# Performance work log

Hardware: AMD Instinct MI355X
Metric: run time of the kernel (lower is better)

Reference implementation:

```python
import jax, jax.numpy as jnp
import numpy as np

TILE = 16            # TILE_WIDTH == TILE_HEIGHT in the Taichi kernel
H, W = 512, 512
TV, TU = H // TILE, W // TILE
NT = TV * TU         # number of 16x16 tiles
PPT = 64             # depth-sorted points assigned to each tile (uniform/padded)
N = NT * PPT


def setup_inputs() -> dict:
    key = jax.random.key(0)
    ks = jax.random.split(key, 7)
    # each tile owns a contiguous depth-sorted chunk of the global point list
    tile_of_point = jnp.arange(N) // PPT
    tu = (tile_of_point % TU).astype(jnp.float32)
    tv = (tile_of_point // TU).astype(jnp.float32)
    center = jnp.stack([tu * TILE + TILE / 2, tv * TILE + TILE / 2], -1)
    point_uv = center + jax.random.normal(ks[0], (N, 2)) * 6.0
    # conic = inverse 2x2 covariance packed as [a, b, c]; keep positive definite
    a = jax.random.uniform(ks[1], (N,), minval=0.02, maxval=0.3)
    c = jax.random.uniform(ks[2], (N,), minval=0.02, maxval=0.3)
    b = jax.random.uniform(ks[3], (N,), minval=-0.5, maxval=0.5) * jnp.sqrt(a * c)
    point_uv_conic = jnp.stack([a, b, c], -1)
    point_alpha_after_activation = jax.random.uniform(ks[4], (N,))
    point_color = jax.random.uniform(ks[5], (N, 3))
    # depths sorted within each tile chunk (front-to-back order, as after radix sort)
    point_depth = jnp.sort(
        jax.random.uniform(ks[6], (N,), minval=0.5, maxval=50.0).reshape(NT, PPT), axis=-1
    ).reshape(N)
    tile_point_indices = jnp.arange(N, dtype=jnp.int32).reshape(NT, PPT)
    return dict(point_uv=point_uv, point_uv_conic=point_uv_conic,
                point_alpha_after_activation=point_alpha_after_activation,
                point_color=point_color, point_depth=point_depth,
                tile_point_indices=tile_point_indices,
                camera_height=H, camera_width=W)


def _to_image(x, tv, tu):
    # x: [NT, TILE*TILE, ...] -> [H, W, ...] (tiles row-major, pixels row-major in tile)
    rest = x.shape[2:]
    x = x.reshape(tv, tu, TILE, TILE, *rest)
    x = jnp.swapaxes(x, 1, 2)
    return x.reshape(tv * TILE, tu * TILE, *rest)


def reference(point_uv, point_uv_conic, point_alpha_after_activation, point_color,
              point_depth, tile_point_indices, camera_height, camera_width):
    TU_ = camera_width // TILE
    TV_ = camera_height // TILE
    NT_ = TU_ * TV_
    PPT_ = tile_point_indices.shape[1]
    # gather per-tile point attributes: [NT, PPT, ...]
    g_uv = point_uv[tile_point_indices]
    g_conic = point_uv_conic[tile_point_indices]
    g_alpha = point_alpha_after_activation[tile_point_indices]
    g_color = point_color[tile_point_indices]
    g_depth = point_depth[tile_point_indices]
    # pixel centers for every tile: [NT, 256]
    p = jnp.arange(TILE * TILE)
    tid = jnp.arange(NT_)
    pix_u = (tid % TU_)[:, None].astype(jnp.float32) * TILE + (p % TILE).astype(jnp.float32)[None, :] + 0.5
    pix_v = (tid // TU_)[:, None].astype(jnp.float32) * TILE + (p // TILE).astype(jnp.float32)[None, :] + 0.5
    # Gaussian density from conic: exp(-0.5*(a dx^2 + c dy^2) - b dx dy)  [NT, 256, PPT]
    dx = pix_u[:, :, None] - g_uv[:, None, :, 0]
    dy = pix_v[:, :, None] - g_uv[:, None, :, 1]
    ca = g_conic[:, None, :, 0]; cb = g_conic[:, None, :, 1]; cc = g_conic[:, None, :, 2]
    dens = jnp.exp(-0.5 * (ca * dx * dx + cc * dy * dy) - cb * dx * dy)
    alpha = dens * g_alpha[:, None, :]
    visible = alpha >= 1.0 / 255.0           # kernel: continue if alpha < 1/255
    alpha_c = jnp.where(visible, jnp.minimum(alpha, 0.99), 0.0)
    one_m = 1.0 - alpha_c
    cp = jnp.cumprod(one_m, axis=-1)
    Ti = jnp.concatenate([jnp.ones_like(cp[..., :1]), cp[..., :-1]], axis=-1)  # exclusive transmittance
    # point whose next_T < 1e-4 saturates the pixel and is itself skipped
    trigger = visible & (Ti * one_m < 1e-4)
    saturated = jnp.cumsum(trigger.astype(jnp.int32), axis=-1) > 0
    contributes = visible & ~saturated
    w = jnp.where(contributes, alpha_c * Ti, 0.0)   # per-point compositing weight
    acc_color = jnp.einsum('tpk,tkc->tpc', w, g_color)
    norm = jnp.sum(w, axis=-1)
    acc_depth = jnp.sum(w * g_depth[:, None, :], axis=-1)
    T_final = jnp.prod(jnp.where(contributes, one_m, 1.0), axis=-1)
    valid_count = jnp.sum(contributes, axis=-1).astype(jnp.int32)
    j = jnp.arange(PPT_, dtype=jnp.int32)
    last = jnp.max(jnp.where(contributes, j[None, None, :] + 1, 0), axis=-1)
    last_offset = (jnp.arange(NT_, dtype=jnp.int32) * PPT_)[:, None] + last
    rasterized_image = _to_image(acc_color, TV_, TU_)
    rasterized_depth = _to_image(acc_depth / jnp.maximum(norm, 1e-6), TV_, TU_)
    pixel_accumulated_alpha = _to_image(1.0 - T_final, TV_, TU_)
    pixel_offset_of_last_effective_point = _to_image(last_offset, TV_, TU_)
    pixel_valid_point_count = _to_image(valid_count, TV_, TU_)
    return (rasterized_image, rasterized_depth, pixel_accumulated_alpha,
            pixel_offset_of_last_effective_point, pixel_valid_point_count)
```

## Files before the change

### kernel.cpp

```cpp
#include <hip/hip_runtime.h>

#define TILE 16
#define PPT 64

#if __has_builtin(__builtin_amdgcn_exp2f)
#define EXP2F(x) __builtin_amdgcn_exp2f(x)
#else
#define EXP2F(x) exp2f(x)
#endif

__device__ __forceinline__ int read_dim(const int* p) {
    int v = *p;
    if (v >= TILE && v <= 65536 && (v % TILE) == 0) return v;
    float f = __int_as_float(v);
    return (int)f;
}

struct Acc {
    float T, Tg, r, g, b, d;
    int cnt, last;
};

__device__ __forceinline__ void step(
    float e, float alpha, const float4& C, int jp1, Acc& a)
{
    const bool  vis   = e >= -7.9943533f;
    const float one_m = fmaxf(1.0f - alpha, 0.01f);
    const float Tone  = a.Tg * one_m;
    const bool  contrib = vis && (Tone >= 1e-4f);
    const float w = contrib ? (a.Tg - Tone) : 0.0f;
    a.r = fmaf(w, C.x, a.r);  a.g = fmaf(w, C.y, a.g);
    a.b = fmaf(w, C.z, a.b);  a.d = fmaf(w, C.w, a.d);
    a.cnt += contrib;
    a.last = contrib ? jp1 : a.last;
    a.T  = contrib ? Tone : a.T;
    a.Tg = vis ? (contrib ? Tone : 0.0f) : a.Tg;
}

__global__ __launch_bounds__(128, 2) void gsplat_raster_kernel(
    const float* __restrict__ point_uv,
    const float* __restrict__ point_conic,
    const float* __restrict__ point_alpha,
    const float* __restrict__ point_color,
    const float* __restrict__ point_depth,
    const int*   __restrict__ tile_point_indices,
    const int*   __restrict__ cam_h_p,
    const int*   __restrict__ cam_w_p,
    float* __restrict__ out)
{
    const int t = blockIdx.x;
    const int p = threadIdx.x;

    const int W  = read_dim(cam_w_p);
    const int H  = read_dim(cam_h_p);
    const int TU = W / TILE;
    const int n_pix = H * W;

    __shared__ float4 sA[PPT];
    __shared__ float2 sB[PPT];
    __shared__ float4 sC[PPT];

    const float L2E = 1.4426950408889634f;
    if (p < PPT) {
        const int gi = tile_point_indices[t * PPT + p];
        const float2 uv = ((const float2*)point_uv)[gi];
        sA[p] = make_float4(uv.x, uv.y,
                            -0.5f * L2E * point_conic[gi * 3 + 0],
                            -0.5f * L2E * point_conic[gi * 3 + 2]);
        sB[p] = make_float2(-L2E * point_conic[gi * 3 + 1],
                            __log2f(point_alpha[gi]));
    } else {
        const int q  = p - PPT;
        const int gi = tile_point_indices[t * PPT + q];
        sC[q] = make_float4(point_color[gi * 3 + 0],
                            point_color[gi * 3 + 1],
                            point_color[gi * 3 + 2],
                            point_depth[gi]);
    }
    __syncthreads();

    const int tu  = t % TU;
    const int tv  = t / TU;
    const int pu  = p % TILE;
    const int pv0 = p / TILE;
    const float pix_u  = (float)(tu * TILE + pu) + 0.5f;
    const float pix_v0 = (float)(tv * TILE + pv0) + 0.5f;

    Acc a0 = {1.0f, 1.0f, 0.f, 0.f, 0.f, 0.f, 0, 0};
    Acc a1 = {1.0f, 1.0f, 0.f, 0.f, 0.f, 0.f, 0, 0};

    #pragma unroll 1
    for (int sg = 0; sg < PPT / 16; ++sg) {
        #pragma unroll
        for (int h = 0; h < 2; ++h) {
            const int gb = sg * 16 + h * 8;

            float  e0[8], e1[8], al0[8], al1[8];
            float4 C[8];
            #pragma unroll
            for (int k = 0; k < 8; ++k) {
                const int j = gb + k;
                const float4 A = sA[j];
                const float2 B = sB[j];
                C[k] = sC[j];
                const float dx   = pix_u - A.x;
                const float q    = B.x * dx;
                const float base = fmaf(A.z * dx, dx, B.y);
                const float dy0  = pix_v0 - A.y;
                const float dy1  = dy0 + 8.0f;
                e0[k] = fmaf(fmaf(A.w, dy0, q), dy0, base);
                e1[k] = fmaf(fmaf(A.w, dy1, q), dy1, base);
                al0[k] = EXP2F(e0[k]);
                al1[k] = EXP2F(e1[k]);
            }

            #pragma unroll
            for (int k = 0; k < 8; ++k) {
                const int jp1 = gb + k + 1;
                step(e0[k], al0[k], C[k], jp1, a0);
                step(e1[k], al1[k], C[k], jp1, a1);
            }
        }
        if (__all((a0.Tg == 0.0f) && (a1.Tg == 0.0f))) break;
    }

    const int c    = tu * TILE + pu;
    const int row0 = tv * TILE + pv0;
    const int pix0 = row0 * W + c;
    const int pix1 = pix0 + 8 * W;

    const float norm0 = 1.0f - a0.T;
    const float norm1 = 1.0f - a1.T;

    out[pix0 * 3 + 0] = a0.r;
    out[pix0 * 3 + 1] = a0.g;
    out[pix0 * 3 + 2] = a0.b;
    out[n_pix * 3 + pix0] = a0.d / fmaxf(norm0, 1e-6f);
    out[n_pix * 4 + pix0] = norm0;
    out[n_pix * 5 + pix0] = (float)(t * PPT + a0.last);
    out[n_pix * 6 + pix0] = (float)a0.cnt;

    out[pix1 * 3 + 0] = a1.r;
    out[pix1 * 3 + 1] = a1.g;
    out[pix1 * 3 + 2] = a1.b;
    out[n_pix * 3 + pix1] = a1.d / fmaxf(norm1, 1e-6f);
    out[n_pix * 4 + pix1] = norm1;
    out[n_pix * 5 + pix1] = (float)(t * PPT + a1.last);
    out[n_pix * 6 + pix1] = (float)a1.cnt;
}

extern "C" void kernel_launch(void* const* d_in, const int* in_sizes, int n_in,
                              void* d_out, int out_size, void* d_ws, size_t ws_size,
                              hipStream_t stream) {
    const float* point_uv    = (const float*)d_in[0];
    const float* point_conic = (const float*)d_in[1];
    const float* point_alpha = (const float*)d_in[2];
    const float* point_color = (const float*)d_in[3];
    const float* point_depth = (const float*)d_in[4];
    const int*   tpi         = (const int*)d_in[5];
    const int*   cam_h       = (const int*)d_in[6];
    const int*   cam_w       = (const int*)d_in[7];

    const int NT = in_sizes[5] / PPT;

    gsplat_raster_kernel<<<NT, 128, 0, stream>>>(
        point_uv, point_conic, point_alpha, point_color, point_depth,
        tpi, cam_h, cam_w, (float*)d_out);
}
```

Measured before the change: 18.45 us.

## Pack color/depth as half2 in shared memory, simplify step logic, check saturation every 8 points

Color and depth are converted to fp16 and packed with the conic b term and log-alpha into one float4 per point, so each point takes two 16-byte LDS reads instead of three. The compositing step is rewritten so contribution is derived from a positive weight and transmittance updates are keyed on the trigger flag, which removes some selects. The early-exit check now runs after every 8 points instead of every 16. The cost is fp16 rounding of color and depth, which may exceed the tolerance for depth values up to 50, and more frequent wave votes.

```diff
diff --git a/kernel.cpp b/kernel.cpp
--- a/kernel.cpp
+++ b/kernel.cpp
@@ -1,4 +1,5 @@
 #include <hip/hip_runtime.h>
+#include <hip/hip_fp16.h>
 
 #define TILE 16
 #define PPT 64
@@ -25,16 +26,19 @@
     float e, float alpha, const float4& C, int jp1, Acc& a)
 {
     const bool  vis   = e >= -7.9943533f;
-    const float one_m = fmaxf(1.0f - alpha, 0.01f);
-    const float Tone  = a.Tg * one_m;
-    const bool  contrib = vis && (Tone >= 1e-4f);
-    const float w = contrib ? (a.Tg - Tone) : 0.0f;
+    const float ag    = vis ? alpha : 0.0f;
+    const float om    = fmaxf(1.0f - ag, 0.01f);
+    const float Tone  = a.Tg * om;
+    const bool  ntrig = Tone >= 1e-4f;
+    const float diff  = a.Tg - Tone;
+    const float w     = ntrig ? diff : 0.0f;
+    const bool  contrib = w > 0.0f;
     a.r = fmaf(w, C.x, a.r);  a.g = fmaf(w, C.y, a.g);
     a.b = fmaf(w, C.z, a.b);  a.d = fmaf(w, C.w, a.d);
     a.cnt += contrib;
     a.last = contrib ? jp1 : a.last;
-    a.T  = contrib ? Tone : a.T;
-    a.Tg = vis ? (contrib ? Tone : 0.0f) : a.Tg;
+    a.T  = ntrig ? Tone : a.T;
+    a.Tg = ntrig ? Tone : 0.0f;
 }
 
 __global__ __launch_bounds__(128, 2) void gsplat_raster_kernel(
@@ -56,26 +60,27 @@
     const int TU = W / TILE;
     const int n_pix = H * W;
 
-    __shared__ float4 sA[PPT];
-    __shared__ float2 sB[PPT];
-    __shared__ float4 sC[PPT];
+    __shared__ float4 sAB[PPT];
+    __shared__ float4 sCD[PPT];
 
     const float L2E = 1.4426950408889634f;
     if (p < PPT) {
         const int gi = tile_point_indices[t * PPT + p];
         const float2 uv = ((const float2*)point_uv)[gi];
-        sA[p] = make_float4(uv.x, uv.y,
-                            -0.5f * L2E * point_conic[gi * 3 + 0],
-                            -0.5f * L2E * point_conic[gi * 3 + 2]);
-        sB[p] = make_float2(-L2E * point_conic[gi * 3 + 1],
-                            __log2f(point_alpha[gi]));
+        sAB[p] = make_float4(uv.x, uv.y,
+                             -0.5f * L2E * point_conic[gi * 3 + 0],
+                             -0.5f * L2E * point_conic[gi * 3 + 2]);
     } else {
         const int q  = p - PPT;
         const int gi = tile_point_indices[t * PPT + q];
-        sC[q] = make_float4(point_color[gi * 3 + 0],
-                            point_color[gi * 3 + 1],
-                            point_color[gi * 3 + 2],
-                            point_depth[gi]);
+        const __half2 rg = __floats2half2_rn(point_color[gi * 3 + 0],
+                                             point_color[gi * 3 + 1]);
+        const __half2 bd = __floats2half2_rn(point_color[gi * 3 + 2],
+                                             point_depth[gi]);
+        sCD[q] = make_float4(-L2E * point_conic[gi * 3 + 1],
+                             __log2f(point_alpha[gi]),
+                             __builtin_bit_cast(float, rg),
+                             __builtin_bit_cast(float, bd));
     }
     __syncthreads();
 
@@ -90,37 +95,38 @@
     Acc a1 = {1.0f, 1.0f, 0.f, 0.f, 0.f, 0.f, 0, 0};
 
     #pragma unroll 1
-    for (int sg = 0; sg < PPT / 16; ++sg) {
+    for (int g = 0; g < PPT / 8; ++g) {
+        const int gb = g * 8;
+
+        float  e0[8], e1[8], al0[8], al1[8];
+        float4 C[8];
         #pragma unroll
-        for (int h = 0; h < 2; ++h) {
-            const int gb = sg * 16 + h * 8;
+        for (int k = 0; k < 8; ++k) {
+            const int j = gb + k;
+            const float4 A = sAB[j];
+            const float4 D = sCD[j];
+            const float dx   = pix_u - A.x;
+            const float q    = D.x * dx;
+            const float base = fmaf(A.z * dx, dx, D.y);
+            const float dy0  = pix_v0 - A.y;
+            const float dy1  = dy0 + 8.0f;
+            e0[k] = fmaf(fmaf(A.w, dy0, q), dy0, base);
+            e1[k] = fmaf(fmaf(A.w, dy1, q), dy1, base);
+            al0[k] = EXP2F(e0[k]);
+            al1[k] = EXP2F(e1[k]);
+            const __half2 rg = __builtin_bit_cast(__half2, D.z);
+            const __half2 bd = __builtin_bit_cast(__half2, D.w);
+            C[k] = make_float4(__low2float(rg), __high2float(rg),
+                               __low2float(bd), __high2float(bd));
+        }
 
-            float  e0[8], e1[8], al0[8], al1[8];
-            float4 C[8];
-            #pragma unroll
-            for (int k = 0; k < 8; ++k) {
-                const int j = gb + k;
-                const float4 A = sA[j];
-                const float2 B = sB[j];
-                C[k] = sC[j];
-                const float dx   = pix_u - A.x;
-                const float q    = B.x * dx;
-                const float base = fmaf(A.z * dx, dx, B.y);
-                const float dy0  = pix_v0 - A.y;
-                const float dy1  = dy0 + 8.0f;
-                e0[k] = fmaf(fmaf(A.w, dy0, q), dy0, base);
-                e1[k] = fmaf(fmaf(A.w, dy1, q), dy1, base);
-                al0[k] = EXP2F(e0[k]);
-                al1[k] = EXP2F(e1[k]);
-            }
+        #pragma unroll
+        for (int k = 0; k < 8; ++k) {
+            const int jp1 = gb + k + 1;
+            step(e0[k], al0[k], C[k], jp1, a0);
+            step(e1[k], al1[k], C[k], jp1, a1);
+        }
 
-            #pragma unroll
-            for (int k = 0; k < 8; ++k) {
-                const int jp1 = gb + k + 1;
-                step(e0[k], al0[k], C[k], jp1, a0);
-                step(e1[k], al1[k], C[k], jp1, a1);
-            }
-        }
         if (__all((a0.Tg == 0.0f) && (a1.Tg == 0.0f))) break;
     }
 
```

Result: slower. 19.45 us (+5.4%).

## Replace serial transmittance chain with parallel prefix products over 8-point groups

Applied to the files above, without the earlier changes.

Invisible points now get a one-minus-alpha factor of 1, and each group of 8 points builds a tree-style prefix product of those factors. The accumulation then multiplies the group's starting transmittance by each prefix instead of running a serial multiply chain, which shortens the dependency chain and exposes instruction-level parallelism. Contribution is detected by a positive weight and saturation by a threshold on the running product. The cost is extra multiplies and possible floating-point differences from reassociation. Semantics at saturation depend on the prefix staying below the threshold, which holds because the product is monotone.

```diff
diff --git a/kernel.cpp b/kernel.cpp
--- a/kernel.cpp
+++ b/kernel.cpp
@@ -16,25 +16,38 @@
     return (int)f;
 }
 
-struct Acc {
-    float T, Tg, r, g, b, d;
-    int cnt, last;
-};
+__device__ __forceinline__ void prefix8(const float om[8], float P[8]) {
+    const float m01 = om[0] * om[1], m23 = om[2] * om[3];
+    const float m45 = om[4] * om[5], m67 = om[6] * om[7];
+    const float m03 = m01 * m23;
+    const float t6  = m45 * om[6];
+    const float m47 = m45 * m67;
+    P[0] = om[0];        P[1] = m01;
+    P[2] = m01 * om[2];  P[3] = m03;
+    P[4] = m03 * om[4];  P[5] = m03 * m45;
+    P[6] = m03 * t6;     P[7] = m03 * m47;
+}
 
-__device__ __forceinline__ void step(
-    float e, float alpha, const float4& C, int jp1, Acc& a)
+__device__ __forceinline__ void group8(
+    const float P[8], const float4 C[8], int gb,
+    float& Tg, float& T, float& ar, float& ag, float& ab, float& ad,
+    int& cnt, int& last)
 {
-    const bool  vis   = e >= -7.9943533f;
-    const float one_m = fmaxf(1.0f - alpha, 0.01f);
-    const float Tone  = a.Tg * one_m;
-    const bool  contrib = vis && (Tone >= 1e-4f);
-    const float w = contrib ? (a.Tg - Tone) : 0.0f;
-    a.r = fmaf(w, C.x, a.r);  a.g = fmaf(w, C.y, a.g);
-    a.b = fmaf(w, C.z, a.b);  a.d = fmaf(w, C.w, a.d);
-    a.cnt += contrib;
-    a.last = contrib ? jp1 : a.last;
-    a.T  = contrib ? Tone : a.T;
-    a.Tg = vis ? (contrib ? Tone : 0.0f) : a.Tg;
+    float Tprev = Tg;
+    #pragma unroll
+    for (int k = 0; k < 8; ++k) {
+        const float Tone  = Tg * P[k];
+        const bool  ntrig = Tone >= 1e-4f;
+        const float w     = ntrig ? (Tprev - Tone) : 0.0f;
+        ar = fmaf(w, C[k].x, ar);  ag = fmaf(w, C[k].y, ag);
+        ab = fmaf(w, C[k].z, ab);  ad = fmaf(w, C[k].w, ad);
+        const bool contrib = w > 0.0f;
+        cnt += contrib;
+        last = contrib ? gb + k + 1 : last;
+        T = contrib ? Tone : T;
+        Tprev = Tone;
+    }
+    Tg = (Tprev >= 1e-4f) ? Tprev : 0.0f;
 }
 
 __global__ __launch_bounds__(128, 2) void gsplat_raster_kernel(
@@ -86,8 +99,9 @@
     const float pix_u  = (float)(tu * TILE + pu) + 0.5f;
     const float pix_v0 = (float)(tv * TILE + pv0) + 0.5f;
 
-    Acc a0 = {1.0f, 1.0f, 0.f, 0.f, 0.f, 0.f, 0, 0};
-    Acc a1 = {1.0f, 1.0f, 0.f, 0.f, 0.f, 0.f, 0, 0};
+    float T0 = 1.0f, Tg0 = 1.0f, r0 = 0.f, g0 = 0.f, b0 = 0.f, d0 = 0.f;
+    float T1 = 1.0f, Tg1 = 1.0f, r1 = 0.f, g1 = 0.f, b1 = 0.f, d1 = 0.f;
+    int cnt0 = 0, cnt1 = 0, last0 = 0, last1 = 0;
 
     #pragma unroll 1
     for (int sg = 0; sg < PPT / 16; ++sg) {
@@ -95,7 +109,7 @@
         for (int h = 0; h < 2; ++h) {
             const int gb = sg * 16 + h * 8;
 
-            float  e0[8], e1[8], al0[8], al1[8];
+            float  om0[8], om1[8];
             float4 C[8];
             #pragma unroll
             for (int k = 0; k < 8; ++k) {
@@ -108,20 +122,21 @@
                 const float base = fmaf(A.z * dx, dx, B.y);
                 const float dy0  = pix_v0 - A.y;
                 const float dy1  = dy0 + 8.0f;
-                e0[k] = fmaf(fmaf(A.w, dy0, q), dy0, base);
-                e1[k] = fmaf(fmaf(A.w, dy1, q), dy1, base);
-                al0[k] = EXP2F(e0[k]);
-                al1[k] = EXP2F(e1[k]);
+                const float al0  = EXP2F(fmaf(fmaf(A.w, dy0, q), dy0, base));
+                const float al1  = EXP2F(fmaf(fmaf(A.w, dy1, q), dy1, base));
+                om0[k] = (al0 >= 1.0f / 255.0f)
+                           ? fmaxf(1.0f - al0, 0.01f) : 1.0f;
+                om1[k] = (al1 >= 1.0f / 255.0f)
+                           ? fmaxf(1.0f - al1, 0.01f) : 1.0f;
             }
 
-            #pragma unroll
-            for (int k = 0; k < 8; ++k) {
-                const int jp1 = gb + k + 1;
-                step(e0[k], al0[k], C[k], jp1, a0);
-                step(e1[k], al1[k], C[k], jp1, a1);
-            }
+            float P0[8], P1[8];
+            prefix8(om0, P0);
+            prefix8(om1, P1);
+            group8(P0, C, gb, Tg0, T0, r0, g0, b0, d0, cnt0, last0);
+            group8(P1, C, gb, Tg1, T1, r1, g1, b1, d1, cnt1, last1);
         }
-        if (__all((a0.Tg == 0.0f) && (a1.Tg == 0.0f))) break;
+        if (__all((Tg0 == 0.0f) && (Tg1 == 0.0f))) break;
     }
 
     const int c    = tu * TILE + pu;
@@ -129,24 +144,24 @@
     const int pix0 = row0 * W + c;
     const int pix1 = pix0 + 8 * W;
 
-    const float norm0 = 1.0f - a0.T;
-    const float norm1 = 1.0f - a1.T;
+    const float norm0 = 1.0f - T0;
+    const float norm1 = 1.0f - T1;
 
-    out[pix0 * 3 + 0] = a0.r;
-    out[pix0 * 3 + 1] = a0.g;
-    out[pix0 * 3 + 2] = a0.b;
-    out[n_pix * 3 + pix0] = a0.d / fmaxf(norm0, 1e-6f);
+    out[pix0 * 3 + 0] = r0;
+    out[pix0 * 3 + 1] = g0;
+    out[pix0 * 3 + 2] = b0;
+    out[n_pix * 3 + pix0] = d0 / fmaxf(norm0, 1e-6f);
     out[n_pix * 4 + pix0] = norm0;
-    out[n_pix * 5 + pix0] = (float)(t * PPT + a0.last);
-    out[n_pix * 6 + pix0] = (float)a0.cnt;
+    out[n_pix * 5 + pix0] = (float)(t * PPT + last0);
+    out[n_pix * 6 + pix0] = (float)cnt0;
 
-    out[pix1 * 3 + 0] = a1.r;
-    out[pix1 * 3 + 1] = a1.g;
-    out[pix1 * 3 + 2] = a1.b;
-    out[n_pix * 3 + pix1] = a1.d / fmaxf(norm1, 1e-6f);
+    out[pix1 * 3 + 0] = r1;
+    out[pix1 * 3 + 1] = g1;
+    out[pix1 * 3 + 2] = b1;
+    out[n_pix * 3 + pix1] = d1 / fmaxf(norm1, 1e-6f);
     out[n_pix * 4 + pix1] = norm1;
-    out[n_pix * 5 + pix1] = (float)(t * PPT + a1.last);
-    out[n_pix * 6 + pix1] = (float)a1.cnt;
+    out[n_pix * 5 + pix1] = (float)(t * PPT + last1);
+    out[n_pix * 6 + pix1] = (float)cnt1;
 }
 
 extern "C" void kernel_launch(void* const* d_in, const int* in_sizes, int n_in,
```

Result: no change. 18.35 us (-0.6%).
